# Performance work log

Hardware: AMD Instinct MI355X
Metric: run time of the kernel (lower is better)

Reference implementation:

```python
import jax, jax.numpy as jnp
import numpy as np

N = 50000
E = 800000
T = 5            # towers
F = 10           # in_num / F_in per tower (divide_input=False)
F_OUT = 2        # out_channels // towers
G = 64           # number of graphs in the batch
L = 2            # conv layers
BN_EPS = 1e-5
STD_EPS = 1e-5


def setup_inputs() -> dict:
    key = jax.random.key(0)
    ks = jax.random.split(key, 24)
    s = 0.1
    inp = {
        'x': jax.random.normal(ks[0], (N, F), jnp.float32),
        'edge_emb': jax.random.normal(ks[1], (4, F), jnp.float32) * s,
        'mlp1_w1': jax.random.normal(ks[2], (F, 5), jnp.float32) * s,
        'mlp1_b1': jnp.zeros((5,), jnp.float32),
        'mlp1_w2': jax.random.normal(ks[3], (5, F), jnp.float32) * s,
        'mlp1_b2': jnp.zeros((F,), jnp.float32),
        'enc_w': jax.random.normal(ks[4], (L, F, F), jnp.float32) * s,
        'enc_b': jnp.zeros((L, F), jnp.float32),
        'pre_w': jax.random.normal(ks[5], (L, T, 3 * F, F), jnp.float32) * s,
        'pre_b': jnp.zeros((L, T, F), jnp.float32),
        'post_w': jax.random.normal(ks[6], (L, T, 13 * F, F_OUT), jnp.float32) * s,
        'post_b': jnp.zeros((L, T, F_OUT), jnp.float32),
        'lin_w': jax.random.normal(ks[7], (L, F, F), jnp.float32) * s,
        'lin_b': jnp.zeros((L, F), jnp.float32),
        'bn_gamma': jnp.ones((L, F), jnp.float32),
        'bn_beta': jnp.zeros((L, F), jnp.float32),
        'mlp2_w1': jax.random.normal(ks[8], (F, 5), jnp.float32) * s,
        'mlp2_b1': jnp.zeros((5,), jnp.float32),
        'mlp2_w2': jax.random.normal(ks[9], (5, 1), jnp.float32) * s,
        'mlp2_b2': jnp.zeros((1,), jnp.float32),
        'edge_index': jax.random.randint(ks[10], (2, E), 0, N, jnp.int64),
        'edge_attr': jax.random.randint(ks[11], (E,), 0, 4, jnp.int64),
        'batch': jnp.sort(jax.random.randint(ks[12], (N,), 0, G, jnp.int64)),
    }
    return inp


def reference(x, edge_emb, mlp1_w1, mlp1_b1, mlp1_w2, mlp1_b2,
              enc_w, enc_b, pre_w, pre_b, post_w, post_b, lin_w, lin_b,
              bn_gamma, bn_beta, mlp2_w1, mlp2_b1, mlp2_w2, mlp2_b2,
              edge_index, edge_attr, batch):
    src, dst = edge_index[0], edge_index[1]
    # mlp1: 10 -> 5 -> 10
    h = jax.nn.relu(x @ mlp1_w1 + mlp1_b1) @ mlp1_w2 + mlp1_b2  # [N, F]
    ea = edge_emb[edge_attr]  # [E, F] edge embedding lookup

    # in-degree at target nodes, PNA degree statistics
    deg = jax.ops.segment_sum(jnp.ones((src.shape[0],), h.dtype), dst, num_segments=N)
    d = jnp.clip(deg, 1.0)
    avg_log = jnp.mean(jnp.log(deg + 1.0))  # avg_deg['log'] from degree distribution
    log_d = jnp.log(d + 1.0)
    amp = (log_d / avg_log)[:, None, None]
    att = (avg_log / log_d)[:, None, None]
    has_in = (deg > 0)[:, None, None]
    inv_d = (1.0 / d)[:, None, None]

    for l in range(L):
        e = ea @ enc_w[l] + enc_b[l]  # [E, F]
        # message = pre_nn(cat(x_i, x_j, edge_attr)) per tower (x shared across towers)
        msg_in = jnp.concatenate([h[dst], h[src], e], axis=-1)  # [E, 3F]
        m = jnp.einsum('ef,tfo->eto', msg_in, pre_w[l]) + pre_b[l]  # [E, T, F]
        mean = jax.ops.segment_sum(m, dst, num_segments=N) * inv_d
        mean2 = jax.ops.segment_sum(m * m, dst, num_segments=N) * inv_d
        std = jnp.sqrt(jax.nn.relu(mean2 - mean * mean) + STD_EPS)
        mn = jnp.where(has_in, jax.ops.segment_min(m, dst, num_segments=N), 0.0)
        mx = jnp.where(has_in, jax.ops.segment_max(m, dst, num_segments=N), 0.0)
        agg = jnp.concatenate([mean, mn, mx, std], axis=-1)  # [N, T, 4F]
        agg = jnp.concatenate([agg, agg * amp, agg * att], axis=-1)  # [N, T, 12F]
        xt = jnp.broadcast_to(h[:, None, :], (h.shape[0], T, F))
        o = jnp.concatenate([xt, agg], axis=-1)  # [N, T, 13F]
        o = jnp.einsum('ntf,tfo->nto', o, post_w[l]) + post_b[l]  # [N, T, F_OUT]
        o = o.reshape(o.shape[0], T * F_OUT) @ lin_w[l] + lin_b[l]  # [N, F]
        # train-mode BatchNorm over nodes
        mu = jnp.mean(o, axis=0)
        var = jnp.var(o, axis=0)
        o = (o - mu) / jnp.sqrt(var + BN_EPS) * bn_gamma[l] + bn_beta[l]
        h = jax.nn.relu(o)

    g = jax.ops.segment_sum(h, batch, num_segments=G)  # global_add_pool -> [G, F]
    out = jax.nn.relu(g @ mlp2_w1 + mlp2_b1) @ mlp2_w2 + mlp2_b2  # [G, 1]
    return out
```

## Files before the change

### kernel.cpp

```cpp
#include <hip/hip_runtime.h>
#include <math.h>

#define N_NODES 50000
#define N_EDGES 800000
#define G_GRAPHS 64
#define CONV_BLOCKS 2048
#define BSTRIDE 64

#define WAVE_SYNC() asm volatile("s_waitcnt lgkmcnt(0)" ::: "memory")
#define RFL(v) __builtin_amdgcn_readfirstlane(v)

__global__ __launch_bounds__(256) void k_mlp1(
    const float* __restrict__ x,
    const float* __restrict__ w1, const float* __restrict__ b1,
    const float* __restrict__ w2, const float* __restrict__ b2,
    float* __restrict__ h,
    int* __restrict__ cnt,
    float* __restrict__ bn_part, float* __restrict__ g_rep,
    float* __restrict__ avg_log,
    const float* __restrict__ edge_emb,
    const float* __restrict__ enc_w, const float* __restrict__ enc_b,
    const float* __restrict__ pre_w, float* __restrict__ encm,
    float* __restrict__ u) {
  __shared__ float eo[2][4][10];
  __shared__ float sw[500];
  __shared__ float hrow[256][11];
  int tid = threadIdx.x;
  int n = blockIdx.x * blockDim.x + tid;
  if (n < 1280) bn_part[n] = 0.f;
  if (n < 32 * G_GRAPHS * 10) g_rep[n] = 0.f;
  if (n == 0) avg_log[0] = 0.f;

  bool act = n < N_NODES;
  if (act) {
    cnt[n] = 0;
    float xv[10];
#pragma unroll
    for (int k = 0; k < 10; k++) xv[k] = x[n * 10 + k];
    float hid[5];
#pragma unroll
    for (int j = 0; j < 5; j++) {
      float a = b1[j];
#pragma unroll
      for (int k = 0; k < 10; k++) a += xv[k] * w1[k * 5 + j];
      hid[j] = fmaxf(a, 0.f);
    }
#pragma unroll
    for (int f = 0; f < 10; f++) {
      float a = b2[f];
#pragma unroll
      for (int j = 0; j < 5; j++) a += hid[j] * w2[j * 10 + f];
      hrow[tid][f] = a;
      h[n * 10 + f] = a;
    }
  }
  for (int j = tid; j < 500; j += 256) {
    int t = j / 100, k = (j / 10) % 10, f = j % 10;
    sw[j] = pre_w[(t * 30 + 10 + k) * 10 + f];
  }
  if (blockIdx.x == 0) {
    for (int i = tid; i < 80; i += 256) {
      int l = i / 40; int a = (i / 10) % 4; int k = i % 10;
      float s = enc_b[l * 10 + k];
      for (int j = 0; j < 10; j++) s += edge_emb[a * 10 + j] * enc_w[(l * 10 + j) * 10 + k];
      eo[l][a][k] = s;
    }
  }
  __syncthreads();
  if (blockIdx.x == 0) {
    for (int i = tid; i < 400; i += 256) {
      int l = i / 200; int a = (i / 50) % 4; int t = (i / 10) % 5; int f = i % 10;
      float s = 0.f;
      for (int k = 0; k < 10; k++) s += eo[l][a][k] * pre_w[((l * 5 + t) * 30 + 20 + k) * 10 + f];
      encm[i] = s;
    }
  }
  int n0 = blockIdx.x * 256;
  int nodesv = N_NODES - n0; if (nodesv > 256) nodesv = 256;
  if (nodesv > 0) {
    int jmax = nodesv * 50;
    for (int j = tid; j < jmax; j += 256) {
      int node = j / 50, c = j % 50;
      int t = c / 10, f2 = c % 10;
      float acc = 0.f;
#pragma unroll
      for (int k = 0; k < 10; k++) acc += hrow[node][k] * sw[t * 100 + f2 + k * 10];
      u[(size_t)n0 * 50 + j] = acc;
    }
  }
}

__global__ void k_scatter(const int* __restrict__ src, const int* __restrict__ dst,
                          const int* __restrict__ attr,
                          int* __restrict__ cnt, int* __restrict__ epk) {
  int e = blockIdx.x * blockDim.x + threadIdx.x;
  if (e >= N_EDGES) return;
  int d = dst[e];
  int s = src[e];
  int a = attr[e];
  int k = atomicAdd(&cnt[d], 1);
  if (k < BSTRIDE) epk[d * BSTRIDE + k] = s | (a << 16);
}

__global__ void k_avg(const int* __restrict__ cnt, float* __restrict__ avg_log) {
  __shared__ float ws[4];
  int tid = threadIdx.x;
  float acc = 0.f;
  for (int n = blockIdx.x * 256 + tid; n < N_NODES; n += gridDim.x * 256)
    acc += __logf((float)cnt[n] + 1.f);
#pragma unroll
  for (int d = 32; d >= 1; d >>= 1) acc += __shfl_down(acc, d, 64);
  if ((tid & 63) == 0) ws[tid >> 6] = acc;
  __syncthreads();
  if (tid == 0) atomicAdd(avg_log, ws[0] + ws[1] + ws[2] + ws[3]);
}

__global__ __launch_bounds__(256) void k_conv(
    const float* __restrict__ h,
    const float* __restrict__ u,
    const float* __restrict__ pre_w_l,
    const float* __restrict__ pre_b_l,
    const float* __restrict__ post_w_l,
    const float* __restrict__ post_b_l,
    const float* __restrict__ lin_w_l,
    const float* __restrict__ lin_b_l,
    const float* __restrict__ encm_l,
    const int* __restrict__ cnt,
    const int* __restrict__ epk,
    const float* __restrict__ avg_log_p,
    float* __restrict__ o_buf,
    float* __restrict__ bn_part)
{
  __shared__ float sW[1300];
  __shared__ float sLin[100];
  __shared__ float sLb[10];
  __shared__ float sPb[10];
  __shared__ float sP[4][100];
  __shared__ float sO[4][10];
  __shared__ float bnS[10], bnQ[10];

  int tid = threadIdx.x;
  int wid = tid >> 6, lane = tid & 63;
  for (int i = tid; i < 1300; i += 256) sW[i] = post_w_l[i];
  for (int i = tid; i < 100; i += 256) sLin[i] = lin_w_l[i];
  if (tid < 10) {
    sLb[tid] = lin_b_l[tid];
    sPb[tid] = post_b_l[tid];
    bnS[tid] = 0.f; bnQ[tid] = 0.f;
  }
  __syncthreads();

  int f = lane % 10;
  int t = (lane < 50) ? (lane / 10) : 4;
  int c50 = t * 10 + f;
  float wdst[10];
#pragma unroll
  for (int k = 0; k < 10; k++) wdst[k] = pre_w_l[(t * 30 + k) * 10 + f];
  float em0 = encm_l[c50];
  float em1 = encm_l[50 + c50];
  float em2 = encm_l[100 + c50];
  float em3 = encm_l[150 + c50];
  float preb = pre_b_l[c50];
  float avg_log = avg_log_p[0] * (1.f / N_NODES);

  int gw = blockIdx.x * 4 + wid;
  int GW = gridDim.x * 4;
  int nn = (gw < N_NODES) ? ((N_NODES - 1 - gw) / GW + 1) : 0;

  int dgp = 0;
  if (lane < nn) dgp = cnt[gw + lane * GW];

  float bnSv = 0.f, bnQv = 0.f;

#define PRE(US, AS, IDX) { int sp_ = __builtin_amdgcn_readlane(pk, (IDX) & 63); \
    AS = sp_ >> 16; US = 0.f; \
    if ((IDX) < deg) US = u[(sp_ & 0xFFFF) * 50 + c50]; }
#define PROC(US, AS) { float em_ = (AS & 2) ? ((AS & 1) ? em3 : em2) : ((AS & 1) ? em1 : em0); \
    float m_ = base + em_ + US; \
    sum += m_; sq = fmaf(m_, m_, sq); mnv = fminf(mnv, m_); mxv = fmaxf(mxv, m_); }

  int nxt_pk = 0;
  if (nn > 0) {
    int deg0 = RFL(__builtin_amdgcn_readlane(dgp, 0));
    if (deg0 > BSTRIDE) deg0 = BSTRIDE;
    if (lane < deg0) nxt_pk = epk[gw * BSTRIDE + lane];
  }

  for (int i = 0; i < nn; i++) {
    int n = gw + i * GW;
    int deg = RFL(__builtin_amdgcn_readlane(dgp, i));
    if (deg > BSTRIDE) deg = BSTRIDE;
    int pk = nxt_pk;
    if (i + 1 < nn) {
      int degN = RFL(__builtin_amdgcn_readlane(dgp, i + 1));
      if (degN > BSTRIDE) degN = BSTRIDE;
      int nN = gw + (i + 1) * GW;
      nxt_pk = (lane < degN) ? epk[nN * BSTRIDE + lane] : 0;
    }

    const float* hn = h + n * 10;
    float2 d0 = *(const float2*)hn;
    float2 d1 = *(const float2*)(hn + 2);
    float2 d2 = *(const float2*)(hn + 4);
    float2 d3 = *(const float2*)(hn + 6);
    float2 d4 = *(const float2*)(hn + 8);
    float xf = hn[f];
    float base = preb
      + d0.x * wdst[0] + d0.y * wdst[1] + d1.x * wdst[2] + d1.y * wdst[3]
      + d2.x * wdst[4] + d2.y * wdst[5] + d3.x * wdst[6] + d3.y * wdst[7]
      + d4.x * wdst[8] + d4.y * wdst[9];

    float sum = 0.f, sq = 0.f, mnv = INFINITY, mxv = -INFINITY;
    {
      float u0, u1, u2, u3, u4, u5, u6, u7;
      int a0, a1, a2, a3, a4, a5, a6, a7;
      PRE(u0, a0, 0) PRE(u1, a1, 1) PRE(u2, a2, 2) PRE(u3, a3, 3)
      PRE(u4, a4, 4) PRE(u5, a5, 5) PRE(u6, a6, 6) PRE(u7, a7, 7)
      int full = deg & ~7;
      int jb = 0;
      for (; jb < full; jb += 8) {
        PROC(u0, a0) PRE(u0, a0, jb + 8)
        PROC(u1, a1) PRE(u1, a1, jb + 9)
        PROC(u2, a2) PRE(u2, a2, jb + 10)
        PROC(u3, a3) PRE(u3, a3, jb + 11)
        PROC(u4, a4) PRE(u4, a4, jb + 12)
        PROC(u5, a5) PRE(u5, a5, jb + 13)
        PROC(u6, a6) PRE(u6, a6, jb + 14)
        PROC(u7, a7) PRE(u7, a7, jb + 15)
      }
      if (jb + 0 < deg) PROC(u0, a0)
      if (jb + 1 < deg) PROC(u1, a1)
      if (jb + 2 < deg) PROC(u2, a2)
      if (jb + 3 < deg) PROC(u3, a3)
      if (jb + 4 < deg) PROC(u4, a4)
      if (jb + 5 < deg) PROC(u5, a5)
      if (jb + 6 < deg) PROC(u6, a6)
    }

    float degf = (float)deg;
    float d = fmaxf(degf, 1.f);
    float inv = 1.f / d;
    float mean = sum * inv;
    float var = sq * inv - mean * mean;
    float stdv = sqrtf(fmaxf(var, 0.f) + 1e-5f);
    if (deg == 0) { mnv = 0.f; mxv = 0.f; }
    float log_d = logf(d + 1.f);
    float amp = log_d / avg_log;
    float att = avg_log / log_d;

    float vv[13];
    vv[0] = xf;
    vv[1] = mean;       vv[2] = mnv;        vv[3] = mxv;        vv[4] = stdv;
    vv[5] = mean * amp; vv[6] = mnv * amp;  vv[7] = mxv * amp;  vv[8] = stdv * amp;
    vv[9] = mean * att; vv[10] = mnv * att; vv[11] = mxv * att; vv[12] = stdv * att;
    float p0 = 0.f, p1 = 0.f;
#pragma unroll
    for (int j = 0; j < 13; j++) {
      const float2 w = *(const float2*)&sW[t * 260 + (f + 10 * j) * 2];
      p0 += vv[j] * w.x; p1 += vv[j] * w.y;
    }
    if (lane < 50) *(float2*)&sP[wid][c50 * 2] = make_float2(p0, p1);
    WAVE_SYNC();
    if (lane < 10) {
      int tt = lane >> 1, c = lane & 1;
      float o = sPb[lane];
#pragma unroll
      for (int ff = 0; ff < 10; ff++) o += sP[wid][(tt * 10 + ff) * 2 + c];
      sO[wid][lane] = o;
    }
    WAVE_SYNC();
    if (lane < 10) {
      float r = sLb[lane];
#pragma unroll
      for (int j = 0; j < 10; j++) r += sO[wid][j] * sLin[j * 10 + lane];
      o_buf[n * 10 + lane] = r;
      bnSv += r; bnQv += r * r;
    }
    WAVE_SYNC();
  }
#undef PRE
#undef PROC

  if (lane < 10) {
    atomicAdd(&bnS[lane], bnSv);
    atomicAdd(&bnQ[lane], bnQv);
  }
  __syncthreads();
  if (tid < 20) {
    float v = (tid < 10) ? bnS[tid] : bnQ[tid - 10];
    atomicAdd(&bn_part[(blockIdx.x & 31) * 20 + tid], v);
  }
}

__global__ __launch_bounds__(256) void k_bnpool(
    const float* __restrict__ o_buf,
    const float* __restrict__ bn_part,
    const float* __restrict__ gamma, const float* __restrict__ beta,
    float* __restrict__ h,
    const int* __restrict__ batch, float* __restrict__ g_rep,
    const float* __restrict__ pre_w_next, float* __restrict__ u,
    int do_u, int do_pool) {
  __shared__ float sS[20];
  __shared__ float sMu[10], sInv[10];
  __shared__ float pool[8][10];
  __shared__ float hrow[25][10];
  __shared__ float sw[500];
  __shared__ int g0s;
  int tid = threadIdx.x;
  int n0 = blockIdx.x * 25;
  int rep = (blockIdx.x & 31) * G_GRAPHS * 10;
  if (do_u) {
    for (int j = tid; j < 500; j += 256) {
      int t = j / 100, k = (j / 10) % 10, f = j % 10;
      sw[j] = pre_w_next[(t * 30 + 10 + k) * 10 + f];
    }
  }
  if (tid < 20) {
    float s = 0.f;
    for (int j = 0; j < 32; j++) s += bn_part[j * 20 + tid];
    sS[tid] = s;
  }
  if (tid < 80) pool[tid / 10][tid % 10] = 0.f;
  if (tid == 0) g0s = batch[n0];
  __syncthreads();
  if (tid < 10) {
    float mu = sS[tid] * (1.f / N_NODES);
    float var = sS[10 + tid] * (1.f / N_NODES) - mu * mu;
    sMu[tid] = mu;
    sInv[tid] = 1.f / sqrtf(fmaxf(var, 0.f) + 1e-5f);
  }
  __syncthreads();
  if (tid < 250) {
    int dn = tid / 10, f = tid % 10;
    int n = n0 + dn;
    int i = n * 10 + f;
    float o = (o_buf[i] - sMu[f]) * sInv[f] * gamma[f] + beta[f];
    float r = fmaxf(o, 0.f);
    h[i] = r;
    hrow[dn][f] = r;
    if (do_pool) {
      int dg = batch[n] - g0s;
      if (dg < 8) atomicAdd(&pool[dg][f], r);
      else atomicAdd(&g_rep[rep + (g0s + dg) * 10 + f], r);
    }
  }
  __syncthreads();
  if (do_u && tid < 250) {
#pragma unroll
    for (int it = 0; it < 5; it++) {
      int j = tid + it * 250;
      int node = j / 50, c = j % 50;
      int t = c / 10, f2 = c % 10;
      float acc = 0.f;
#pragma unroll
      for (int k = 0; k < 10; k++) acc += hrow[node][k] * sw[t * 100 + f2 + k * 10];
      u[n0 * 50 + j] = acc;
    }
  }
  if (do_pool) {
    __syncthreads();
    if (tid < 80) {
      float v = pool[tid / 10][tid % 10];
      if (v != 0.f) atomicAdd(&g_rep[rep + (g0s + tid / 10) * 10 + tid % 10], v);
    }
  }
}

__global__ void k_mlp2(const float* __restrict__ g_rep,
                       const float* __restrict__ w1, const float* __restrict__ b1,
                       const float* __restrict__ w2, const float* __restrict__ b2,
                       float* __restrict__ out) {
  int b = threadIdx.x;
  if (b >= G_GRAPHS) return;
  float gv[10];
#pragma unroll
  for (int k = 0; k < 10; k++) gv[k] = 0.f;
  for (int r = 0; r < 32; r++) {
#pragma unroll
    for (int k = 0; k < 10; k++) gv[k] += g_rep[r * G_GRAPHS * 10 + b * 10 + k];
  }
  float acc = b2[0];
#pragma unroll
  for (int j = 0; j < 5; j++) {
    float a = b1[j];
#pragma unroll
    for (int k = 0; k < 10; k++) a += gv[k] * w1[k * 5 + j];
    acc += fmaxf(a, 0.f) * w2[j];
  }
  out[b] = acc;
}

extern "C" void kernel_launch(void* const* d_in, const int* in_sizes, int n_in,
                              void* d_out, int out_size, void* d_ws, size_t ws_size,
                              hipStream_t stream) {
  const float* x        = (const float*)d_in[0];
  const float* edge_emb = (const float*)d_in[1];
  const float* m1w1 = (const float*)d_in[2];
  const float* m1b1 = (const float*)d_in[3];
  const float* m1w2 = (const float*)d_in[4];
  const float* m1b2 = (const float*)d_in[5];
  const float* enc_w = (const float*)d_in[6];
  const float* enc_b = (const float*)d_in[7];
  const float* pre_w = (const float*)d_in[8];
  const float* pre_b = (const float*)d_in[9];
  const float* post_w = (const float*)d_in[10];
  const float* post_b = (const float*)d_in[11];
  const float* lin_w = (const float*)d_in[12];
  const float* lin_b = (const float*)d_in[13];
  const float* bn_g = (const float*)d_in[14];
  const float* bn_b = (const float*)d_in[15];
  const float* m2w1 = (const float*)d_in[16];
  const float* m2b1 = (const float*)d_in[17];
  const float* m2w2 = (const float*)d_in[18];
  const float* m2b2 = (const float*)d_in[19];
  const int* edge_index = (const int*)d_in[20];
  const int* edge_attr  = (const int*)d_in[21];
  const int* batch      = (const int*)d_in[22];
  const int* src  = edge_index;
  const int* dstp = edge_index + N_EDGES;

  char* ws = (char*)d_ws;
  size_t off = 0;
  auto alloc = [&](size_t bytes) {
    void* p = ws + off;
    off += (bytes + 255) & ~(size_t)255;
    return p;
  };
  float*     h       = (float*)alloc(N_NODES * 10 * sizeof(float));
  float*     o_buf   = (float*)alloc(N_NODES * 10 * sizeof(float));
  float*     u       = (float*)alloc((size_t)(N_NODES * 50 + 64) * sizeof(float));
  int*       cnt     = (int*)alloc(N_NODES * sizeof(int));
  int*       epk     = (int*)alloc((size_t)N_NODES * BSTRIDE * sizeof(int));
  float*     encm    = (float*)alloc(400 * sizeof(float));
  float*     avg_log = (float*)alloc(16);
  float*     bn_part = (float*)alloc(2 * 32 * 20 * sizeof(float));
  float*     g_rep   = (float*)alloc(32 * G_GRAPHS * 10 * sizeof(float));

  k_mlp1<<<(N_NODES + 255) / 256, 256, 0, stream>>>(x, m1w1, m1b1, m1w2, m1b2, h,
                                                    cnt, bn_part, g_rep, avg_log,
                                                    edge_emb, enc_w, enc_b, pre_w, encm, u);
  k_scatter<<<(N_EDGES + 255) / 256, 256, 0, stream>>>(src, dstp, edge_attr, cnt, epk);
  k_avg<<<64, 256, 0, stream>>>(cnt, avg_log);

  for (int l = 0; l < 2; l++) {
    k_conv<<<CONV_BLOCKS, 256, 0, stream>>>(
        h, u, pre_w + l * 1500, pre_b + l * 50, post_w + l * 1300, post_b + l * 10,
        lin_w + l * 100, lin_b + l * 10, encm + l * 200,
        cnt, epk, avg_log, o_buf, bn_part + l * 640);
    k_bnpool<<<N_NODES / 25, 256, 0, stream>>>(
        o_buf, bn_part + l * 640, bn_g + l * 10, bn_b + l * 10, h, batch, g_rep,
        pre_w + 1500, u, l == 0, l == 1);
  }
  k_mlp2<<<1, 64, 0, stream>>>(g_rep, m2w1, m2b1, m2w2, m2b2, (float*)d_out);
}
```

Before: 295.4 us.

## Fuse whole pipeline into one persistent cooperative kernel with grid syncs

Merges the mlp1, scatter, degree-average, two conv layers, batchnorm/pool and final MLP stages into a single cooperatively launched persistent kernel. Stages are separated by grid-wide barriers, and grid-stride loops replace the per-stage launch geometry. The aim is to remove the per-launch gaps and tail effects between the eight small kernels. In exchange it adds grid.sync costs, raises shared-memory use per block, which can limit occupancy, and ties the grid size to occupancy. The old multi-kernel path is kept as a fallback if the cooperative launch fails.

```diff
diff --git a/kernel.cpp b/kernel.cpp
--- a/kernel.cpp
+++ b/kernel.cpp
@@ -1,145 +1,31 @@
 #include <hip/hip_runtime.h>
+#include <hip/hip_cooperative_groups.h>
 #include <math.h>
+
+namespace cg = cooperative_groups;
 
 #define N_NODES 50000
 #define N_EDGES 800000
 #define G_GRAPHS 64
+#define NTHR 256
+#define BSTRIDE 64
 #define CONV_BLOCKS 2048
-#define BSTRIDE 64
 
 #define WAVE_SYNC() asm volatile("s_waitcnt lgkmcnt(0)" ::: "memory")
 #define RFL(v) __builtin_amdgcn_readfirstlane(v)
 
-__global__ __launch_bounds__(256) void k_mlp1(
-    const float* __restrict__ x,
-    const float* __restrict__ w1, const float* __restrict__ b1,
-    const float* __restrict__ w2, const float* __restrict__ b2,
-    float* __restrict__ h,
-    int* __restrict__ cnt,
-    float* __restrict__ bn_part, float* __restrict__ g_rep,
-    float* __restrict__ avg_log,
-    const float* __restrict__ edge_emb,
-    const float* __restrict__ enc_w, const float* __restrict__ enc_b,
-    const float* __restrict__ pre_w, float* __restrict__ encm,
-    float* __restrict__ u) {
-  __shared__ float eo[2][4][10];
-  __shared__ float sw[500];
-  __shared__ float hrow[256][11];
-  int tid = threadIdx.x;
-  int n = blockIdx.x * blockDim.x + tid;
-  if (n < 1280) bn_part[n] = 0.f;
-  if (n < 32 * G_GRAPHS * 10) g_rep[n] = 0.f;
-  if (n == 0) avg_log[0] = 0.f;
-
-  bool act = n < N_NODES;
-  if (act) {
-    cnt[n] = 0;
-    float xv[10];
-#pragma unroll
-    for (int k = 0; k < 10; k++) xv[k] = x[n * 10 + k];
-    float hid[5];
-#pragma unroll
-    for (int j = 0; j < 5; j++) {
-      float a = b1[j];
-#pragma unroll
-      for (int k = 0; k < 10; k++) a += xv[k] * w1[k * 5 + j];
-      hid[j] = fmaxf(a, 0.f);
-    }
-#pragma unroll
-    for (int f = 0; f < 10; f++) {
-      float a = b2[f];
-#pragma unroll
-      for (int j = 0; j < 5; j++) a += hid[j] * w2[j * 10 + f];
-      hrow[tid][f] = a;
-      h[n * 10 + f] = a;
-    }
-  }
-  for (int j = tid; j < 500; j += 256) {
-    int t = j / 100, k = (j / 10) % 10, f = j % 10;
-    sw[j] = pre_w[(t * 30 + 10 + k) * 10 + f];
-  }
-  if (blockIdx.x == 0) {
-    for (int i = tid; i < 80; i += 256) {
-      int l = i / 40; int a = (i / 10) % 4; int k = i % 10;
-      float s = enc_b[l * 10 + k];
-      for (int j = 0; j < 10; j++) s += edge_emb[a * 10 + j] * enc_w[(l * 10 + j) * 10 + k];
-      eo[l][a][k] = s;
-    }
-  }
-  __syncthreads();
-  if (blockIdx.x == 0) {
-    for (int i = tid; i < 400; i += 256) {
-      int l = i / 200; int a = (i / 50) % 4; int t = (i / 10) % 5; int f = i % 10;
-      float s = 0.f;
-      for (int k = 0; k < 10; k++) s += eo[l][a][k] * pre_w[((l * 5 + t) * 30 + 20 + k) * 10 + f];
-      encm[i] = s;
-    }
-  }
-  int n0 = blockIdx.x * 256;
-  int nodesv = N_NODES - n0; if (nodesv > 256) nodesv = 256;
-  if (nodesv > 0) {
-    int jmax = nodesv * 50;
-    for (int j = tid; j < jmax; j += 256) {
-      int node = j / 50, c = j % 50;
-      int t = c / 10, f2 = c % 10;
-      float acc = 0.f;
-#pragma unroll
-      for (int k = 0; k < 10; k++) acc += hrow[node][k] * sw[t * 100 + f2 + k * 10];
-      u[(size_t)n0 * 50 + j] = acc;
-    }
-  }
-}
-
-__global__ void k_scatter(const int* __restrict__ src, const int* __restrict__ dst,
-                          const int* __restrict__ attr,
-                          int* __restrict__ cnt, int* __restrict__ epk) {
-  int e = blockIdx.x * blockDim.x + threadIdx.x;
-  if (e >= N_EDGES) return;
-  int d = dst[e];
-  int s = src[e];
-  int a = attr[e];
-  int k = atomicAdd(&cnt[d], 1);
-  if (k < BSTRIDE) epk[d * BSTRIDE + k] = s | (a << 16);
-}
-
-__global__ void k_avg(const int* __restrict__ cnt, float* __restrict__ avg_log) {
-  __shared__ float ws[4];
-  int tid = threadIdx.x;
-  float acc = 0.f;
-  for (int n = blockIdx.x * 256 + tid; n < N_NODES; n += gridDim.x * 256)
-    acc += __logf((float)cnt[n] + 1.f);
-#pragma unroll
-  for (int d = 32; d >= 1; d >>= 1) acc += __shfl_down(acc, d, 64);
-  if ((tid & 63) == 0) ws[tid >> 6] = acc;
-  __syncthreads();
-  if (tid == 0) atomicAdd(avg_log, ws[0] + ws[1] + ws[2] + ws[3]);
-}
-
-__global__ __launch_bounds__(256) void k_conv(
-    const float* __restrict__ h,
-    const float* __restrict__ u,
-    const float* __restrict__ pre_w_l,
-    const float* __restrict__ pre_b_l,
-    const float* __restrict__ post_w_l,
-    const float* __restrict__ post_b_l,
-    const float* __restrict__ lin_w_l,
-    const float* __restrict__ lin_b_l,
+__device__ __forceinline__ void conv_body(
+    int gw, int GW, int tid, float avg_log,
+    const float* __restrict__ h, const float* __restrict__ u,
+    const float* __restrict__ pre_w_l, const float* __restrict__ pre_b_l,
+    const float* __restrict__ post_w_l, const float* __restrict__ post_b_l,
+    const float* __restrict__ lin_w_l, const float* __restrict__ lin_b_l,
     const float* __restrict__ encm_l,
-    const int* __restrict__ cnt,
-    const int* __restrict__ epk,
-    const float* __restrict__ avg_log_p,
-    float* __restrict__ o_buf,
-    float* __restrict__ bn_part)
+    const int* __restrict__ cnt, const int* __restrict__ epk,
+    float* __restrict__ o_buf, float* __restrict__ bn_part_l, int bnslot,
+    float* sW, float* sLin, float* sLb, float* sPb,
+    float (*sP)[100], float (*sO)[10], float* bnS, float* bnQ)
 {
-  __shared__ float sW[1300];
-  __shared__ float sLin[100];
-  __shared__ float sLb[10];
-  __shared__ float sPb[10];
-  __shared__ float sP[4][100];
-  __shared__ float sO[4][10];
-  __shared__ float bnS[10], bnQ[10];
-
-  int tid = threadIdx.x;
   int wid = tid >> 6, lane = tid & 63;
   for (int i = tid; i < 1300; i += 256) sW[i] = post_w_l[i];
   for (int i = tid; i < 100; i += 256) sLin[i] = lin_w_l[i];
@@ -161,10 +47,7 @@
   float em2 = encm_l[100 + c50];
   float em3 = encm_l[150 + c50];
   float preb = pre_b_l[c50];
-  float avg_log = avg_log_p[0] * (1.f / N_NODES);
-
-  int gw = blockIdx.x * 4 + wid;
-  int GW = gridDim.x * 4;
+
   int nn = (gw < N_NODES) ? ((N_NODES - 1 - gw) / GW + 1) : 0;
 
   int dgp = 0;
@@ -288,16 +171,370 @@
   __syncthreads();
   if (tid < 20) {
     float v = (tid < 10) ? bnS[tid] : bnQ[tid - 10];
-    atomicAdd(&bn_part[(blockIdx.x & 31) * 20 + tid], v);
-  }
+    atomicAdd(&bn_part_l[bnslot * 20 + tid], v);
+  }
+}
+
+__global__ __launch_bounds__(256, 4) void k_all(
+    const float* __restrict__ x,
+    const float* __restrict__ m1w1, const float* __restrict__ m1b1,
+    const float* __restrict__ m1w2, const float* __restrict__ m1b2,
+    float* __restrict__ h, int* __restrict__ cnt,
+    float* __restrict__ bn_part, float* __restrict__ g_rep,
+    float* __restrict__ avg_log,
+    const float* __restrict__ edge_emb,
+    const float* __restrict__ enc_w, const float* __restrict__ enc_b,
+    const float* __restrict__ pre_w, float* __restrict__ encm,
+    float* __restrict__ u,
+    const int* __restrict__ src, const int* __restrict__ dstp,
+    const int* __restrict__ attr, int* __restrict__ epk,
+    const float* __restrict__ pre_b,
+    const float* __restrict__ post_w, const float* __restrict__ post_b,
+    const float* __restrict__ lin_w, const float* __restrict__ lin_b,
+    const float* __restrict__ bn_g, const float* __restrict__ bn_b,
+    const int* __restrict__ batch,
+    const float* __restrict__ m2w1, const float* __restrict__ m2b1,
+    const float* __restrict__ m2w2, const float* __restrict__ m2b2,
+    float* __restrict__ out, float* __restrict__ o_buf)
+{
+  cg::grid_group grid = cg::this_grid();
+  __shared__ float sW[1300];
+  __shared__ float sLin[100];
+  __shared__ float sLb[10], sPb[10];
+  __shared__ float sP[4][100];
+  __shared__ float sO[4][10];
+  __shared__ float bnS[10], bnQ[10];
+  __shared__ float sw[500];
+  __shared__ float hrow[256][11];
+  __shared__ float eo[2][4][10];
+  __shared__ float sS[20], sMu[10], sInv[10];
+  __shared__ float pool[8][10];
+  __shared__ float wred[4];
+  __shared__ int g0s;
+
+  int tid = threadIdx.x;
+  int bid = blockIdx.x;
+  int NB = gridDim.x;
+  int GT = NB * NTHR;
+  int gtid = bid * NTHR + tid;
+
+  if (gtid < 1280) bn_part[gtid] = 0.f;
+  if (gtid < 32 * G_GRAPHS * 10) g_rep[gtid] = 0.f;
+  if (gtid < N_NODES) cnt[gtid] = 0;
+  if (gtid == 0) avg_log[0] = 0.f;
+
+  bool nodeblk = (bid * NTHR) < N_NODES;
+  if (nodeblk) {
+    int n = gtid;
+    if (n < N_NODES) {
+      float xv[10];
+#pragma unroll
+      for (int k = 0; k < 10; k++) xv[k] = x[n * 10 + k];
+      float hid[5];
+#pragma unroll
+      for (int j = 0; j < 5; j++) {
+        float a = m1b1[j];
+#pragma unroll
+        for (int k = 0; k < 10; k++) a += xv[k] * m1w1[k * 5 + j];
+        hid[j] = fmaxf(a, 0.f);
+      }
+#pragma unroll
+      for (int f = 0; f < 10; f++) {
+        float a = m1b2[f];
+#pragma unroll
+        for (int j = 0; j < 5; j++) a += hid[j] * m1w2[j * 10 + f];
+        hrow[tid][f] = a;
+        h[n * 10 + f] = a;
+      }
+    }
+    for (int j = tid; j < 500; j += 256) {
+      int t = j / 100, k = (j / 10) % 10, f = j % 10;
+      sw[j] = pre_w[(t * 30 + 10 + k) * 10 + f];
+    }
+  }
+  if (bid == 0) {
+    for (int i = tid; i < 80; i += 256) {
+      int l = i / 40; int a = (i / 10) % 4; int k = i % 10;
+      float s = enc_b[l * 10 + k];
+      for (int j = 0; j < 10; j++) s += edge_emb[a * 10 + j] * enc_w[(l * 10 + j) * 10 + k];
+      eo[l][a][k] = s;
+    }
+  }
+  __syncthreads();
+  if (bid == 0) {
+    for (int i = tid; i < 400; i += 256) {
+      int l = i / 200; int a = (i / 50) % 4; int t = (i / 10) % 5; int f = i % 10;
+      float s = 0.f;
+      for (int k = 0; k < 10; k++) s += eo[l][a][k] * pre_w[((l * 5 + t) * 30 + 20 + k) * 10 + f];
+      encm[i] = s;
+    }
+  }
+  if (nodeblk) {
+    int n0 = bid * 256;
+    int nodesv = N_NODES - n0; if (nodesv > 256) nodesv = 256;
+    int jmax = nodesv * 50;
+    for (int j = tid; j < jmax; j += 256) {
+      int node = j / 50, c = j % 50;
+      int t = c / 10, f2 = c % 10;
+      float acc = 0.f;
+#pragma unroll
+      for (int k = 0; k < 10; k++) acc += hrow[node][k] * sw[t * 100 + f2 + k * 10];
+      u[(size_t)n0 * 50 + j] = acc;
+    }
+  }
+  grid.sync();
+
+  for (int e = gtid; e < N_EDGES; e += GT) {
+    int d = dstp[e];
+    int s = src[e];
+    int a = attr[e];
+    int k = atomicAdd(&cnt[d], 1);
+    if (k < BSTRIDE) epk[d * BSTRIDE + k] = s | (a << 16);
+  }
+  grid.sync();
+
+  {
+    float acc = 0.f;
+    for (int n2 = gtid; n2 < N_NODES; n2 += GT)
+      acc += __logf((float)cnt[n2] + 1.f);
+#pragma unroll
+    for (int d = 32; d >= 1; d >>= 1) acc += __shfl_down(acc, d, 64);
+    if ((tid & 63) == 0) wred[tid >> 6] = acc;
+    __syncthreads();
+    if (tid == 0) {
+      float s4 = wred[0] + wred[1] + wred[2] + wred[3];
+      if (s4 != 0.f) atomicAdd(avg_log, s4);
+    }
+  }
+  grid.sync();
+  float al = avg_log[0] * (1.f / N_NODES);
+
+  for (int l = 0; l < 2; l++) {
+    conv_body(bid * 4 + (tid >> 6), NB * 4, tid, al, h, u,
+              pre_w + l * 1500, pre_b + l * 50, post_w + l * 1300, post_b + l * 10,
+              lin_w + l * 100, lin_b + l * 10, encm + l * 200,
+              cnt, epk, o_buf, bn_part + l * 640, bid & 31,
+              sW, sLin, sLb, sPb, sP, sO, bnS, bnQ);
+    grid.sync();
+    const float* bn_part_l = bn_part + l * 640;
+    const float* gamma = bn_g + l * 10;
+    const float* beta  = bn_b + l * 10;
+    int do_u = (l == 0), do_pool = (l == 1);
+    if (do_u) {
+      for (int j = tid; j < 500; j += 256) {
+        int t = j / 100, k = (j / 10) % 10, f = j % 10;
+        sw[j] = pre_w[1500 + (t * 30 + 10 + k) * 10 + f];
+      }
+    }
+    if (tid < 20) {
+      float s = 0.f;
+      for (int j = 0; j < 32; j++) s += bn_part_l[j * 20 + tid];
+      sS[tid] = s;
+    }
+    __syncthreads();
+    if (tid < 10) {
+      float mu = sS[tid] * (1.f / N_NODES);
+      float var = sS[10 + tid] * (1.f / N_NODES) - mu * mu;
+      sMu[tid] = mu;
+      sInv[tid] = 1.f / sqrtf(fmaxf(var, 0.f) + 1e-5f);
+    }
+    __syncthreads();
+    for (int vb = bid; vb < N_NODES / 25; vb += NB) {
+      int n0 = vb * 25;
+      int rep = (vb & 31) * G_GRAPHS * 10;
+      if (tid < 80) pool[tid / 10][tid % 10] = 0.f;
+      if (tid == 0) g0s = batch[n0];
+      __syncthreads();
+      if (tid < 250) {
+        int dn = tid / 10, f = tid % 10;
+        int n = n0 + dn;
+        int i = n * 10 + f;
+        float o = (o_buf[i] - sMu[f]) * sInv[f] * gamma[f] + beta[f];
+        float r = fmaxf(o, 0.f);
+        h[i] = r;
+        hrow[dn][f] = r;
+        if (do_pool) {
+          int dg = batch[n] - g0s;
+          if (dg < 8) atomicAdd(&pool[dg][f], r);
+          else atomicAdd(&g_rep[rep + (g0s + dg) * 10 + f], r);
+        }
+      }
+      __syncthreads();
+      if (do_u && tid < 250) {
+#pragma unroll
+        for (int it = 0; it < 5; it++) {
+          int j = tid + it * 250;
+          int node = j / 50, c = j % 50;
+          int t = c / 10, f2 = c % 10;
+          float acc = 0.f;
+#pragma unroll
+          for (int k = 0; k < 10; k++) acc += hrow[node][k] * sw[t * 100 + f2 + k * 10];
+          u[n0 * 50 + j] = acc;
+        }
+      }
+      if (do_pool) {
+        __syncthreads();
+        if (tid < 80) {
+          float v = pool[tid / 10][tid % 10];
+          if (v != 0.f) atomicAdd(&g_rep[rep + (g0s + tid / 10) * 10 + tid % 10], v);
+        }
+      }
+      __syncthreads();
+    }
+    grid.sync();
+  }
+
+  if (bid == 0 && tid < G_GRAPHS) {
+    float gv[10];
+#pragma unroll
+    for (int k = 0; k < 10; k++) gv[k] = 0.f;
+    for (int r = 0; r < 32; r++) {
+#pragma unroll
+      for (int k = 0; k < 10; k++) gv[k] += g_rep[r * G_GRAPHS * 10 + tid * 10 + k];
+    }
+    float acc = m2b2[0];
+#pragma unroll
+    for (int j = 0; j < 5; j++) {
+      float a = m2b1[j];
+#pragma unroll
+      for (int k = 0; k < 10; k++) a += gv[k] * m2w1[k * 5 + j];
+      acc += fmaxf(a, 0.f) * m2w2[j];
+    }
+    out[tid] = acc;
+  }
+}
+
+__global__ __launch_bounds__(256) void k_mlp1(
+    const float* __restrict__ x,
+    const float* __restrict__ w1, const float* __restrict__ b1,
+    const float* __restrict__ w2, const float* __restrict__ b2,
+    float* __restrict__ h, int* __restrict__ cnt,
+    float* __restrict__ bn_part, float* __restrict__ g_rep,
+    float* __restrict__ avg_log,
+    const float* __restrict__ edge_emb,
+    const float* __restrict__ enc_w, const float* __restrict__ enc_b,
+    const float* __restrict__ pre_w, float* __restrict__ encm,
+    float* __restrict__ u) {
+  __shared__ float eo[2][4][10];
+  __shared__ float sw[500];
+  __shared__ float hrow[256][11];
+  int tid = threadIdx.x;
+  int n = blockIdx.x * blockDim.x + tid;
+  if (n < 1280) bn_part[n] = 0.f;
+  if (n < 32 * G_GRAPHS * 10) g_rep[n] = 0.f;
+  if (n == 0) avg_log[0] = 0.f;
+  bool act = n < N_NODES;
+  if (act) {
+    cnt[n] = 0;
+    float xv[10];
+#pragma unroll
+    for (int k = 0; k < 10; k++) xv[k] = x[n * 10 + k];
+    float hid[5];
+#pragma unroll
+    for (int j = 0; j < 5; j++) {
+      float a = b1[j];
+#pragma unroll
+      for (int k = 0; k < 10; k++) a += xv[k] * w1[k * 5 + j];
+      hid[j] = fmaxf(a, 0.f);
+    }
+#pragma unroll
+    for (int f = 0; f < 10; f++) {
+      float a = b2[f];
+#pragma unroll
+      for (int j = 0; j < 5; j++) a += hid[j] * w2[j * 10 + f];
+      hrow[tid][f] = a;
+      h[n * 10 + f] = a;
+    }
+  }
+  for (int j = tid; j < 500; j += 256) {
+    int t = j / 100, k = (j / 10) % 10, f = j % 10;
+    sw[j] = pre_w[(t * 30 + 10 + k) * 10 + f];
+  }
+  if (blockIdx.x == 0) {
+    for (int i = tid; i < 80; i += 256) {
+      int l = i / 40; int a = (i / 10) % 4; int k = i % 10;
+      float s = enc_b[l * 10 + k];
+      for (int j = 0; j < 10; j++) s += edge_emb[a * 10 + j] * enc_w[(l * 10 + j) * 10 + k];
+      eo[l][a][k] = s;
+    }
+  }
+  __syncthreads();
+  if (blockIdx.x == 0) {
+    for (int i = tid; i < 400; i += 256) {
+      int l = i / 200; int a = (i / 50) % 4; int t = (i / 10) % 5; int f = i % 10;
+      float s = 0.f;
+      for (int k = 0; k < 10; k++) s += eo[l][a][k] * pre_w[((l * 5 + t) * 30 + 20 + k) * 10 + f];
+      encm[i] = s;
+    }
+  }
+  int n0 = blockIdx.x * 256;
+  int nodesv = N_NODES - n0; if (nodesv > 256) nodesv = 256;
+  if (nodesv > 0) {
+    int jmax = nodesv * 50;
+    for (int j = tid; j < jmax; j += 256) {
+      int node = j / 50, c = j % 50;
+      int t = c / 10, f2 = c % 10;
+      float acc = 0.f;
+#pragma unroll
+      for (int k = 0; k < 10; k++) acc += hrow[node][k] * sw[t * 100 + f2 + k * 10];
+      u[(size_t)n0 * 50 + j] = acc;
+    }
+  }
+}
+
+__global__ void k_scatter(const int* __restrict__ src, const int* __restrict__ dst,
+                          const int* __restrict__ attr,
+                          int* __restrict__ cnt, int* __restrict__ epk) {
+  int e = blockIdx.x * blockDim.x + threadIdx.x;
+  if (e >= N_EDGES) return;
+  int d = dst[e];
+  int s = src[e];
+  int a = attr[e];
+  int k = atomicAdd(&cnt[d], 1);
+  if (k < BSTRIDE) epk[d * BSTRIDE + k] = s | (a << 16);
+}
+
+__global__ void k_avg(const int* __restrict__ cnt, float* __restrict__ avg_log) {
+  __shared__ float ws[4];
+  int tid = threadIdx.x;
+  float acc = 0.f;
+  for (int n = blockIdx.x * 256 + tid; n < N_NODES; n += gridDim.x * 256)
+    acc += __logf((float)cnt[n] + 1.f);
+#pragma unroll
+  for (int d = 32; d >= 1; d >>= 1) acc += __shfl_down(acc, d, 64);
+  if ((tid & 63) == 0) ws[tid >> 6] = acc;
+  __syncthreads();
+  if (tid == 0) atomicAdd(avg_log, ws[0] + ws[1] + ws[2] + ws[3]);
+}
+
+__global__ __launch_bounds__(256) void k_conv(
+    const float* __restrict__ h, const float* __restrict__ u,
+    const float* __restrict__ pre_w_l, const float* __restrict__ pre_b_l,
+    const float* __restrict__ post_w_l, const float* __restrict__ post_b_l,
+    const float* __restrict__ lin_w_l, const float* __restrict__ lin_b_l,
+    const float* __restrict__ encm_l,
+    const int* __restrict__ cnt, const int* __restrict__ epk,
+    const float* __restrict__ avg_log_p,
+    float* __restrict__ o_buf, float* __restrict__ bn_part)
+{
+  __shared__ float sW[1300];
+  __shared__ float sLin[100];
+  __shared__ float sLb[10], sPb[10];
+  __shared__ float sP[4][100];
+  __shared__ float sO[4][10];
+  __shared__ float bnS[10], bnQ[10];
+  int tid = threadIdx.x;
+  float al = avg_log_p[0] * (1.f / N_NODES);
+  conv_body(blockIdx.x * 4 + (tid >> 6), gridDim.x * 4, tid, al, h, u,
+            pre_w_l, pre_b_l, post_w_l, post_b_l, lin_w_l, lin_b_l, encm_l,
+            cnt, epk, o_buf, bn_part, blockIdx.x & 31,
+            sW, sLin, sLb, sPb, sP, sO, bnS, bnQ);
 }
 
 __global__ __launch_bounds__(256) void k_bnpool(
-    const float* __restrict__ o_buf,
-    const float* __restrict__ bn_part,
+    const float* __restrict__ o_buf, const float* __restrict__ bn_part,
     const float* __restrict__ gamma, const float* __restrict__ beta,
-    float* __restrict__ h,
-    const int* __restrict__ batch, float* __restrict__ g_rep,
+    float* __restrict__ h, const int* __restrict__ batch, float* __restrict__ g_rep,
     const float* __restrict__ pre_w_next, float* __restrict__ u,
     int do_u, int do_pool) {
   __shared__ float sS[20];
@@ -414,7 +651,7 @@
   const float* m2w2 = (const float*)d_in[18];
   const float* m2b2 = (const float*)d_in[19];
   const int* edge_index = (const int*)d_in[20];
-  const int* edge_attr  = (const int*)d_in[21];
+  const int* attr       = (const int*)d_in[21];
   const int* batch      = (const int*)d_in[22];
   const int* src  = edge_index;
   const int* dstp = edge_index + N_EDGES;
@@ -426,30 +663,55 @@
     off += (bytes + 255) & ~(size_t)255;
     return p;
   };
-  float*     h       = (float*)alloc(N_NODES * 10 * sizeof(float));
-  float*     o_buf   = (float*)alloc(N_NODES * 10 * sizeof(float));
-  float*     u       = (float*)alloc((size_t)(N_NODES * 50 + 64) * sizeof(float));
-  int*       cnt     = (int*)alloc(N_NODES * sizeof(int));
-  int*       epk     = (int*)alloc((size_t)N_NODES * BSTRIDE * sizeof(int));
-  float*     encm    = (float*)alloc(400 * sizeof(float));
-  float*     avg_log = (float*)alloc(16);
-  float*     bn_part = (float*)alloc(2 * 32 * 20 * sizeof(float));
-  float*     g_rep   = (float*)alloc(32 * G_GRAPHS * 10 * sizeof(float));
-
-  k_mlp1<<<(N_NODES + 255) / 256, 256, 0, stream>>>(x, m1w1, m1b1, m1w2, m1b2, h,
-                                                    cnt, bn_part, g_rep, avg_log,
-                                                    edge_emb, enc_w, enc_b, pre_w, encm, u);
-  k_scatter<<<(N_EDGES + 255) / 256, 256, 0, stream>>>(src, dstp, edge_attr, cnt, epk);
-  k_avg<<<64, 256, 0, stream>>>(cnt, avg_log);
-
-  for (int l = 0; l < 2; l++) {
-    k_conv<<<CONV_BLOCKS, 256, 0, stream>>>(
-        h, u, pre_w + l * 1500, pre_b + l * 50, post_w + l * 1300, post_b + l * 10,
-        lin_w + l * 100, lin_b + l * 10, encm + l * 200,
-        cnt, epk, avg_log, o_buf, bn_part + l * 640);
-    k_bnpool<<<N_NODES / 25, 256, 0, stream>>>(
-        o_buf, bn_part + l * 640, bn_g + l * 10, bn_b + l * 10, h, batch, g_rep,
-        pre_w + 1500, u, l == 0, l == 1);
-  }
-  k_mlp2<<<1, 64, 0, stream>>>(g_rep, m2w1, m2b1, m2w2, m2b2, (float*)d_out);
-}
+  float* h       = (float*)alloc(N_NODES * 10 * sizeof(float));
+  float* o_buf   = (float*)alloc(N_NODES * 10 * sizeof(float));
+  float* u       = (float*)alloc((size_t)(N_NODES * 50 + 64) * sizeof(float));
+  int*   cnt     = (int*)alloc(N_NODES * sizeof(int));
+  int*   epk     = (int*)alloc((size_t)N_NODES * BSTRIDE * sizeof(int));
+  float* encm    = (float*)alloc(400 * sizeof(float));
+  float* avg_log = (float*)alloc(16);
+  float* bn_part = (float*)alloc(2 * 32 * 20 * sizeof(float));
+  float* g_rep   = (float*)alloc(32 * G_GRAPHS * 10 * sizeof(float));
+  float* outp    = (float*)d_out;
+
+  int perCU = 0;
+  hipError_t occ_err = hipOccupancyMaxActiveBlocksPerMultiprocessor(
+      &perCU, reinterpret_cast<const void*>(k_all), NTHR, 0);
+  int nblk = (occ_err == hipSuccess) ? perCU * 256 : 0;
+  if (nblk > 2048) nblk = 2048;
+
+  bool coop_ok = false;
+  if (nblk >= 256) {
+    void* args[] = {
+      (void*)&x, (void*)&m1w1, (void*)&m1b1, (void*)&m1w2, (void*)&m1b2,
+      (void*)&h, (void*)&cnt, (void*)&bn_part, (void*)&g_rep, (void*)&avg_log,
+      (void*)&edge_emb, (void*)&enc_w, (void*)&enc_b, (void*)&pre_w, (void*)&encm,
+      (void*)&u, (void*)&src, (void*)&dstp, (void*)&attr, (void*)&epk,
+      (void*)&pre_b, (void*)&post_w, (void*)&post_b, (void*)&lin_w, (void*)&lin_b,
+      (void*)&bn_g, (void*)&bn_b, (void*)&batch,
+      (void*)&m2w1, (void*)&m2b1, (void*)&m2w2, (void*)&m2b2,
+      (void*)&outp, (void*)&o_buf
+    };
+    hipError_t e = hipLaunchCooperativeKernel(
+        reinterpret_cast<const void*>(k_all), dim3(nblk), dim3(NTHR), args, 0, stream);
+    coop_ok = (e == hipSuccess);
+  }
+
+  if (!coop_ok) {
+    k_mlp1<<<(N_NODES + 255) / 256, 256, 0, stream>>>(x, m1w1, m1b1, m1w2, m1b2, h,
+                                                      cnt, bn_part, g_rep, avg_log,
+                                                      edge_emb, enc_w, enc_b, pre_w, encm, u);
+    k_scatter<<<(N_EDGES + 255) / 256, 256, 0, stream>>>(src, dstp, attr, cnt, epk);
+    k_avg<<<64, 256, 0, stream>>>(cnt, avg_log);
+    for (int l = 0; l < 2; l++) {
+      k_conv<<<CONV_BLOCKS, 256, 0, stream>>>(
+          h, u, pre_w + l * 1500, pre_b + l * 50, post_w + l * 1300, post_b + l * 10,
+          lin_w + l * 100, lin_b + l * 10, encm + l * 200,
+          cnt, epk, avg_log, o_buf, bn_part + l * 640);
+      k_bnpool<<<N_NODES / 25, 256, 0, stream>>>(
+          o_buf, bn_part + l * 640, bn_g + l * 10, bn_b + l * 10, h, batch, g_rep,
+          pre_w + 1500, u, l == 0, l == 1);
+    }
+    k_mlp2<<<1, 64, 0, stream>>>(g_rep, m2w1, m2b1, m2w2, m2b2, outp);
+  }
+}
```

New measurement: 744.5 us. +152.1%, slower.
